# Kernel tuning notes

Hardware: AMD Instinct MI355X
Metric: run time of the kernel (lower is better)

Reference implementation:

```python
import jax, jax.numpy as jnp
import numpy as np

B, T, D = 32, 256, 1024      # batch, seq_len, input_size
H = D // 2                   # LSTM hidden size = 512
K = 128                      # num_tags


def setup_inputs() -> dict:
    key = jax.random.key(0)
    ks = jax.random.split(key, 16)
    s_in = 1.0 / np.sqrt(D + K)
    s_h = 1.0 / np.sqrt(H)
    return {
        "hiddens": jax.random.normal(ks[0], (B, T, D), jnp.float32),
        "h_t": jax.random.normal(ks[1], (2, B, H), jnp.float32),
        "c_t": jax.random.normal(ks[2], (2, B, H), jnp.float32),
        "mask": jnp.ones((B, T), jnp.float32),
        # output layer: Linear(H, K)
        "W_out": jax.random.normal(ks[3], (K, H), jnp.float32) * s_h,
        "b_out": jnp.zeros((K,), jnp.float32),
        # LSTM layer 0: input dim = K + D
        "W_ih0": jax.random.normal(ks[4], (4 * H, K + D), jnp.float32) * s_in,
        "W_hh0": jax.random.normal(ks[5], (4 * H, H), jnp.float32) * s_h,
        "b_ih0": jnp.zeros((4 * H,), jnp.float32),
        "b_hh0": jnp.zeros((4 * H,), jnp.float32),
        # LSTM layer 1: input dim = H
        "W_ih1": jax.random.normal(ks[6], (4 * H, H), jnp.float32) * s_h,
        "W_hh1": jax.random.normal(ks[7], (4 * H, H), jnp.float32) * s_h,
        "b_ih1": jnp.zeros((4 * H,), jnp.float32),
        "b_hh1": jnp.zeros((4 * H,), jnp.float32),
    }


def _lstm_cell(x, h, c, W_ih, W_hh, b_ih, b_hh):
    g = x @ W_ih.T + h @ W_hh.T + b_ih + b_hh
    i, f, gg, o = jnp.split(g, 4, axis=-1)
    i = jax.nn.sigmoid(i); f = jax.nn.sigmoid(f)
    gg = jnp.tanh(gg); o = jax.nn.sigmoid(o)
    c = f * c + i * gg
    h = o * jnp.tanh(c)
    return h, c


def reference(hiddens, h_t, c_t, mask, W_out, b_out,
              W_ih0, W_hh0, b_ih0, b_hh0, W_ih1, W_hh1, b_ih1, b_hh1):
    # initial previous-tag distribution from first frame's first half
    last_tag = hiddens[:, 0, :H] @ W_out.T + b_out          # [B,K]
    sm = jax.nn.softmax(last_tag, axis=-1)

    def step(carry, x_t):
        h1, c1, h2, c2, sm = carry
        inp = jnp.concatenate([x_t, sm], axis=-1)           # [B, D+K]
        h1, c1 = _lstm_cell(inp, h1, c1, W_ih0, W_hh0, b_ih0, b_hh0)
        h2, c2 = _lstm_cell(h1, h2, c2, W_ih1, W_hh1, b_ih1, b_hh1)
        logit = h2 @ W_out.T + b_out                        # [B,K]
        sm = jax.nn.softmax(logit, axis=-1)
        return (h1, c1, h2, c2, sm), logit

    carry0 = (h_t[0], c_t[0], h_t[1], c_t[1], sm)
    _, logits_t = jax.lax.scan(step, carry0, jnp.swapaxes(hiddens, 0, 1))  # [T,B,K]
    logits = jnp.swapaxes(logits_t, 0, 1)                   # [B,T,K]
    logits = logits + (1.0 - mask)[:, :, None] * jnp.float32(-1e32)
    prob = jax.nn.softmax(logits, axis=-1)
    return prob
```

## Files before the change

### kernel.cpp

```cpp
#include <hip/hip_runtime.h>
#include <cstdint>
#include <cstddef>


#define Bz   32
#define Tz   256
#define Dz   1024
#define Hz   512
#define NK   128
#define IN0  1152
#define NBLK 256
#define BH   16384

typedef float vf4 __attribute__((ext_vector_type(4)));

__device__ __forceinline__ void ldsc4(vf4& d, const float* p) {
  asm volatile("global_load_dwordx4 %0, %1, off sc0 sc1" : "=v"(d) : "v"(p));
}
__device__ __forceinline__ void stsc1(float* p, float v) {
  asm volatile("global_store_dword %0, %1, off sc0 sc1" :: "v"(p), "v"(v) : "memory");
}
#define FENCE8(c, a0,a1,a2,a3,a4,a5,a6,a7) \
  asm volatile("s_waitcnt vmcnt(" #c ")" : "+v"(a0),"+v"(a1),"+v"(a2),"+v"(a3), \
               "+v"(a4),"+v"(a5),"+v"(a6),"+v"(a7) :: "memory")

#define FMA4(acc, W_, A_) \
  acc = fmaf((W_).x,(A_).x, fmaf((W_).y,(A_).y, fmaf((W_).z,(A_).z, fmaf((W_).w,(A_).w,(acc)))))

__device__ __forceinline__ float sigf(float x) { return 1.0f / (1.0f + expf(-x)); }

__device__ __forceinline__ void gbar(unsigned int* bar, unsigned int g) {
  asm volatile("s_waitcnt vmcnt(0)" ::: "memory");
  __syncthreads();
  if (threadIdx.x == 0)
    __hip_atomic_store(bar + blockIdx.x * 16, g,
                       __ATOMIC_RELAXED, __HIP_MEMORY_SCOPE_SYSTEM);
  if (blockIdx.x == NBLK - 1) {
    unsigned int* wsl = bar + threadIdx.x * 16;
    while (__hip_atomic_load(wsl, __ATOMIC_RELAXED, __HIP_MEMORY_SCOPE_SYSTEM) < g)
      __builtin_amdgcn_s_sleep(1);
    __syncthreads();
    if (threadIdx.x == 0) {
      asm volatile("s_waitcnt vmcnt(0)" ::: "memory");
      __hip_atomic_store(bar + NBLK * 16, g,
                         __ATOMIC_RELAXED, __HIP_MEMORY_SCOPE_SYSTEM);
    }
  } else if (threadIdx.x == 0) {
    while (__hip_atomic_load(bar + NBLK * 16, __ATOMIC_RELAXED,
                             __HIP_MEMORY_SCOPE_SYSTEM) < g)
      __builtin_amdgcn_s_sleep(1);
  }
  __syncthreads();
}

#define FMAROW(r, AV, BASE, KOFF) \
  { vf4 wv = *(const vf4*)&BASE[r][KOFF]; FMA4(A##r, wv, AV); }
#define R16A(OP, AV, BASE, KOFF) \
  OP(0,AV,BASE,KOFF) OP(1,AV,BASE,KOFF) OP(2,AV,BASE,KOFF) OP(3,AV,BASE,KOFF) \
  OP(4,AV,BASE,KOFF) OP(5,AV,BASE,KOFF) OP(6,AV,BASE,KOFF) OP(7,AV,BASE,KOFF) \
  OP(8,AV,BASE,KOFF) OP(9,AV,BASE,KOFF) OP(10,AV,BASE,KOFF) OP(11,AV,BASE,KOFF) \
  OP(12,AV,BASE,KOFF) OP(13,AV,BASE,KOFF) OP(14,AV,BASE,KOFF) OP(15,AV,BASE,KOFF)

#define RED16 { \
  { const bool hi = (ks & 1) != 0; \
    float s0=hi?A0:A8, s1=hi?A1:A9, s2=hi?A2:A10, s3=hi?A3:A11; \
    float s4=hi?A4:A12, s5=hi?A5:A13, s6=hi?A6:A14, s7=hi?A7:A15; \
    float k0=hi?A8:A0, k1=hi?A9:A1, k2=hi?A10:A2, k3=hi?A11:A3; \
    float k4=hi?A12:A4, k5=hi?A13:A5, k6=hi?A14:A6, k7=hi?A15:A7; \
    A0=k0+__shfl_xor(s0,1,64); A1=k1+__shfl_xor(s1,1,64); \
    A2=k2+__shfl_xor(s2,1,64); A3=k3+__shfl_xor(s3,1,64); \
    A4=k4+__shfl_xor(s4,1,64); A5=k5+__shfl_xor(s5,1,64); \
    A6=k6+__shfl_xor(s6,1,64); A7=k7+__shfl_xor(s7,1,64); } \
  { const bool hi = (ks & 2) != 0; \
    float s0=hi?A0:A4, s1=hi?A1:A5, s2=hi?A2:A6, s3=hi?A3:A7; \
    float k0=hi?A4:A0, k1=hi?A5:A1, k2=hi?A6:A2, k3=hi?A7:A3; \
    A0=k0+__shfl_xor(s0,2,64); A1=k1+__shfl_xor(s1,2,64); \
    A2=k2+__shfl_xor(s2,2,64); A3=k3+__shfl_xor(s3,2,64); } \
  { const bool hi = (ks & 4) != 0; \
    float s0=hi?A0:A2, s1=hi?A1:A3; float k0=hi?A2:A0, k1=hi?A3:A1; \
    A0=k0+__shfl_xor(s0,4,64); A1=k1+__shfl_xor(s1,4,64); } \
  { const bool hi = (ks & 8) != 0; \
    float s0=hi?A0:A1; float k0=hi?A1:A0; \
    A0=k0+__shfl_xor(s0,8,64); } }

#define ZERO16 A0=0.f;A1=0.f;A2=0.f;A3=0.f;A4=0.f;A5=0.f;A6=0.f;A7=0.f; \
               A8=0.f;A9=0.f;A10=0.f;A11=0.f;A12=0.f;A13=0.f;A14=0.f;A15=0.f;

#define GATES(CREG, HDST) \
  __syncthreads(); \
  if (tid < 64) { \
    float gi = gbuf[cu][cbl],      gf = gbuf[4 + cu][cbl]; \
    float gg = gbuf[8 + cu][cbl],  go = gbuf[12 + cu][cbl]; \
    CREG = sigf(gf) * CREG + sigf(gi) * tanhf(gg); \
    stsc1(HDST + (size_t)(pg * 16 + cbl) * Hz + jg * 4 + cu, \
          sigf(go) * tanhf(CREG)); \
  }

__device__ void c_slot(const float* src, int t, int bb,
                       const float* __restrict__ W_out, const float* __restrict__ b_out,
                       const float* __restrict__ mask,
                       float* __restrict__ smg, float* __restrict__ out,
                       float (*cpart)[2], float* wred) {
  const int tid = threadIdx.x;
  const int n = tid & 127, kh = tid >> 7;
  float p = 0.0f;
  const float* w  = W_out + (size_t)n * Hz + kh * 256;
  const float* s2 = src + kh * 256;
  #pragma unroll 8
  for (int k = 0; k < 256; k += 4) {
    vf4 sv = *(const vf4*)(s2 + k);
    vf4 wv = *(const vf4*)(w + k);
    p += sv.x * wv.x + sv.y * wv.y + sv.z * wv.z + sv.w * wv.w;
  }
  cpart[n][kh] = p;
  __syncthreads();
  float logit = 0.0f;
  if (tid < 128) logit = cpart[n][0] + cpart[n][1] + b_out[n];
  float m = logit;
  #pragma unroll
  for (int off = 32; off >= 1; off >>= 1) m = fmaxf(m, __shfl_xor(m, off));
  if ((tid & 63) == 0 && tid < 128) wred[tid >> 6] = m;
  __syncthreads();
  float M = fmaxf(wred[0], wred[1]);
  float e = (tid < 128) ? expf(logit - M) : 0.0f;
  float s = e;
  #pragma unroll
  for (int off = 32; off >= 1; off >>= 1) s += __shfl_xor(s, off);
  if ((tid & 63) == 0 && tid < 128) wred[2 + (tid >> 6)] = s;
  __syncthreads();
  float S = wred[2] + wred[3];
  if (tid < 128) stsc1(smg + bb * NK + n, e / S);
  if (t >= 0) {
    float mk = (tid < 128) ? mask[bb * Tz + t] : 1.0f;
    float lm = (tid < 128) ? (logit + (1.0f - mk) * (-1e32f)) : -3.0e38f;
    float m2 = lm;
    #pragma unroll
    for (int off = 32; off >= 1; off >>= 1) m2 = fmaxf(m2, __shfl_xor(m2, off));
    if ((tid & 63) == 0 && tid < 128) wred[4 + (tid >> 6)] = m2;
    __syncthreads();
    float M2 = fmaxf(wred[4], wred[5]);
    float e2 = (tid < 128) ? expf(lm - M2) : 0.0f;
    float s2r = e2;
    #pragma unroll
    for (int off = 32; off >= 1; off >>= 1) s2r += __shfl_xor(s2r, off);
    if ((tid & 63) == 0 && tid < 128) wred[6 + (tid >> 6)] = s2r;
    __syncthreads();
    float S2 = wred[6] + wred[7];
    if (tid < 128) out[((size_t)bb * Tz + t) * NK + n] = e2 / S2;
  }
}

__global__ void __launch_bounds__(256)
xpre_kernel(const float* __restrict__ hiddens, const float* __restrict__ W_ih0,
            const float* __restrict__ b_ih0, const float* __restrict__ b_hh0,
            float* __restrict__ Xpre, int t0, int colTiles, int cstride) {
  __shared__ float Ws[16][64];
  __shared__ float Hs[16][64];
  const int tid = threadIdx.x;
  const int bx = blockIdx.x % colTiles;
  const int by = blockIdx.x / colTiles;
  const int n0 = by * 64, c0 = bx * 64;
  const int tx = tid & 15, ty = tid >> 4;
  const int ldn = tid >> 2;
  const int ldk = (tid & 3) * 4;

  const int bb = ldn & 31;
  const int tt = t0 + (c0 >> 5) + (ldn >> 5);
  const float* hsrc = hiddens + ((size_t)bb * Tz + tt) * Dz + ldk;
  const float* wsrc = W_ih0 + (size_t)(n0 + ldn) * IN0 + ldk;

  float acc[4][4] = {};
  vf4 wv = *(const vf4*)(wsrc);
  vf4 hv = *(const vf4*)(hsrc);
  for (int k0 = 0; k0 < Dz; k0 += 16) {
    __syncthreads();
    Ws[ldk + 0][ldn] = wv.x; Ws[ldk + 1][ldn] = wv.y;
    Ws[ldk + 2][ldn] = wv.z; Ws[ldk + 3][ldn] = wv.w;
    Hs[ldk + 0][ldn] = hv.x; Hs[ldk + 1][ldn] = hv.y;
    Hs[ldk + 2][ldn] = hv.z; Hs[ldk + 3][ldn] = hv.w;
    __syncthreads();
    if (k0 + 16 < Dz) {
      wv = *(const vf4*)(wsrc + k0 + 16);
      hv = *(const vf4*)(hsrc + k0 + 16);
    }
    #pragma unroll
    for (int k = 0; k < 16; ++k) {
      vf4 a4 = *(const vf4*)&Ws[k][ty * 4];
      vf4 b4 = *(const vf4*)&Hs[k][tx * 4];
      acc[0][0] += a4.x * b4.x; acc[0][1] += a4.x * b4.y; acc[0][2] += a4.x * b4.z; acc[0][3] += a4.x * b4.w;
      acc[1][0] += a4.y * b4.x; acc[1][1] += a4.y * b4.y; acc[1][2] += a4.y * b4.z; acc[1][3] += a4.y * b4.w;
      acc[2][0] += a4.z * b4.x; acc[2][1] += a4.z * b4.y; acc[2][2] += a4.z * b4.z; acc[2][3] += a4.z * b4.w;
      acc[3][0] += a4.w * b4.x; acc[3][1] += a4.w * b4.y; acc[3][2] += a4.w * b4.z; acc[3][3] += a4.w * b4.w;
    }
  }
  #pragma unroll
  for (int i = 0; i < 4; ++i) {
    int n = n0 + ty * 4 + i;
    float bi = b_ih0[n] + b_hh0[n];
    vf4 v; v.x = acc[i][0] + bi; v.y = acc[i][1] + bi;
    v.z = acc[i][2] + bi; v.w = acc[i][3] + bi;
    *(vf4*)(Xpre + (size_t)n * cstride + c0 + tx * 4) = v;
  }
}

__global__ void __launch_bounds__(256)
seq_kernel(const float* __restrict__ hiddens,
           const float* __restrict__ h_t, const float* __restrict__ c_t,
           const float* __restrict__ mask,
           const float* __restrict__ W_out, const float* __restrict__ b_out,
           const float* __restrict__ W_ih0, const float* __restrict__ W_hh0,
           const float* __restrict__ W_ih1, const float* __restrict__ W_hh1,
           const float* __restrict__ b_ih1, const float* __restrict__ b_hh1,
           const float* __restrict__ Xpre, float* __restrict__ out,
           float* __restrict__ h1g, float* __restrict__ h2g,
           float* __restrict__ smg, float* __restrict__ c1g, float* __restrict__ c2g,
           unsigned int* bar, int t0, int nsteps, int cstride) {
  __shared__ float wA[16][640];
  __shared__ float wB[16][1024];
  __shared__ float gbuf[16][17];
  __shared__ float biasB[16];
  __shared__ float hsg[512];
  __shared__ float cpart[128][2];
  __shared__ float wred[8];

  const int tid = threadIdx.x;
  const int bid = blockIdx.x;
  const int jg  = bid >> 1;
  const int pg  = bid & 1;
  const int ks  = tid & 15;
  const int bbl = tid >> 4;
  const int bbg = pg * 16 + bbl;
  const int ks4 = ks * 4;
  const int cu  = tid & 3, cbl = tid >> 2;
  const int rr  = ((ks & 1) << 3) | ((ks & 2) << 1) | ((ks & 4) >> 1) | ((ks & 8) >> 3);
  const int rowG = ((rr >> 2) * Hz) + jg * 4 + (rr & 3);

  for (int r = 0; r < 16; ++r) {
    const int row = ((r >> 2) * Hz) + jg * 4 + (r & 3);
    if (tid * 4 < 512)
      *(vf4*)&wA[r][tid * 4] = *(const vf4*)(W_hh0 + (size_t)row * Hz + tid * 4);
    if (tid * 4 < 128)
      *(vf4*)&wA[r][512 + tid * 4] = *(const vf4*)(W_ih0 + (size_t)row * IN0 + 1024 + tid * 4);
    if (tid * 4 < 512) {
      *(vf4*)&wB[r][tid * 4]       = *(const vf4*)(W_ih1 + (size_t)row * Hz + tid * 4);
      *(vf4*)&wB[r][512 + tid * 4] = *(const vf4*)(W_hh1 + (size_t)row * Hz + tid * 4);
    }
  }
  if (tid < 16) {
    const int row = ((tid >> 2) * Hz) + jg * 4 + (tid & 3);
    biasB[tid] = b_ih1[row] + b_hh1[row];
  }

  float c1r = 0.0f, c2r = 0.0f;
  if (tid < 64) {
    const size_t ci = (size_t)(pg * 16 + cbl) * Hz + jg * 4 + cu;
    if (t0 == 0) { c1r = c_t[ci]; c2r = c_t[BH + ci]; }
    else         { c1r = c1g[ci]; c2r = c2g[ci]; }
  }

  if (t0 == 0) {
    if (bid < 32 && tid < 128) {
      vf4 v1 = *(const vf4*)(h_t + (size_t)bid * Hz + tid * 4);
      vf4 v2 = *(const vf4*)(h_t + BH + (size_t)bid * Hz + tid * 4);
      float* d1 = h1g + BH + (size_t)bid * Hz + tid * 4;
      float* d2 = h2g + BH + (size_t)bid * Hz + tid * 4;
      stsc1(d1, v1.x); stsc1(d1 + 1, v1.y); stsc1(d1 + 2, v1.z); stsc1(d1 + 3, v1.w);
      stsc1(d2, v2.x); stsc1(d2 + 1, v2.y); stsc1(d2 + 2, v2.z); stsc1(d2 + 3, v2.w);
    }
    if (bid < 32) {
      if (tid < 128)
        *(vf4*)&hsg[tid * 4] = *(const vf4*)(hiddens + (size_t)bid * Tz * Dz + tid * 4);
      __syncthreads();
      c_slot(hsg, -1, bid, W_out, b_out, mask, smg, out, cpart, wred);
    }
  }
  __syncthreads();
  unsigned int g = 1;
  gbar(bar, g); ++g;

  for (int t = t0; t < t0 + nsteps; ++t) {
    const float* h1prev = h1g + ((t + 1) & 1) * BH;
    float*       h1cur  = h1g + (t & 1) * BH;
    const float* h2prev = h2g + ((t + 1) & 1) * BH;
    float*       h2cur  = h2g + (t & 1) * BH;
    float A0,A1,A2,A3,A4,A5,A6,A7,A8,A9,A10,A11,A12,A13,A14,A15;

    {
      vf4 ah0,ah1,ah2,ah3,ah4,ah5,ah6,ah7, as0,as1;
      const float* hp = h1prev + (size_t)bbg * Hz + ks4;
      ldsc4(ah0, hp);        ldsc4(ah1, hp + 64);  ldsc4(ah2, hp + 128);
      ldsc4(ah3, hp + 192);  ldsc4(ah4, hp + 256); ldsc4(ah5, hp + 320);
      ldsc4(ah6, hp + 384);  ldsc4(ah7, hp + 448);
      const float* sp = smg + (size_t)bbg * NK + ks4;
      ldsc4(as0, sp);        ldsc4(as1, sp + 64);
      float xv = Xpre[(size_t)rowG * cstride + (t - t0) * 32 + bbg];
      ZERO16
      FENCE8(3, ah0,ah1,ah2,ah3,ah4,ah5,ah6,ah7);
      R16A(FMAROW, ah0, wA, ks4 +   0)
      R16A(FMAROW, ah1, wA, ks4 +  64)
      R16A(FMAROW, ah2, wA, ks4 + 128)
      R16A(FMAROW, ah3, wA, ks4 + 192)
      R16A(FMAROW, ah4, wA, ks4 + 256)
      R16A(FMAROW, ah5, wA, ks4 + 320)
      R16A(FMAROW, ah6, wA, ks4 + 384)
      R16A(FMAROW, ah7, wA, ks4 + 448)
      asm volatile("s_waitcnt vmcnt(0)" : "+v"(as0), "+v"(as1), "+v"(xv) :: "memory");
      R16A(FMAROW, as0, wA, ks4 + 512)
      R16A(FMAROW, as1, wA, ks4 + 576)
      RED16
      gbuf[rr][bbl] = A0 + xv;
      GATES(c1r, h1cur)
    }
    gbar(bar, g); ++g;

    {
      vf4 aa0,aa1,aa2,aa3,aa4,aa5,aa6,aa7, ab0,ab1,ab2,ab3,ab4,ab5,ab6,ab7;
      const float* p1 = h1cur + (size_t)bbg * Hz + ks4;
      ldsc4(aa0, p1);       ldsc4(aa1, p1 + 64);  ldsc4(aa2, p1 + 128);
      ldsc4(aa3, p1 + 192); ldsc4(aa4, p1 + 256); ldsc4(aa5, p1 + 320);
      ldsc4(aa6, p1 + 384); ldsc4(aa7, p1 + 448);
      const float* p2 = h2prev + (size_t)bbg * Hz + ks4;
      ldsc4(ab0, p2);       ldsc4(ab1, p2 + 64);  ldsc4(ab2, p2 + 128);
      ldsc4(ab3, p2 + 192); ldsc4(ab4, p2 + 256); ldsc4(ab5, p2 + 320);
      ldsc4(ab6, p2 + 384); ldsc4(ab7, p2 + 448);
      ZERO16
      FENCE8(8, aa0,aa1,aa2,aa3,aa4,aa5,aa6,aa7);
      R16A(FMAROW, aa0, wB, ks4 +   0)
      R16A(FMAROW, aa1, wB, ks4 +  64)
      R16A(FMAROW, aa2, wB, ks4 + 128)
      R16A(FMAROW, aa3, wB, ks4 + 192)
      R16A(FMAROW, aa4, wB, ks4 + 256)
      R16A(FMAROW, aa5, wB, ks4 + 320)
      R16A(FMAROW, aa6, wB, ks4 + 384)
      R16A(FMAROW, aa7, wB, ks4 + 448)
      FENCE8(0, ab0,ab1,ab2,ab3,ab4,ab5,ab6,ab7);
      R16A(FMAROW, ab0, wB, ks4 + 512)
      R16A(FMAROW, ab1, wB, ks4 + 576)
      R16A(FMAROW, ab2, wB, ks4 + 640)
      R16A(FMAROW, ab3, wB, ks4 + 704)
      R16A(FMAROW, ab4, wB, ks4 + 768)
      R16A(FMAROW, ab5, wB, ks4 + 832)
      R16A(FMAROW, ab6, wB, ks4 + 896)
      R16A(FMAROW, ab7, wB, ks4 + 960)
      RED16
      gbuf[rr][bbl] = A0 + biasB[rr];
      GATES(c2r, h2cur)
    }
    gbar(bar, g); ++g;

    if (bid < 32) {
      if (tid < 128) {
        vf4 v;
        ldsc4(v, h2cur + (size_t)bid * Hz + tid * 4);
        asm volatile("s_waitcnt vmcnt(0)" : "+v"(v) :: "memory");
        *(vf4*)&hsg[tid * 4] = v;
      }
      __syncthreads();
      c_slot(hsg, t, bid, W_out, b_out, mask, smg, out, cpart, wred);
    }
    gbar(bar, g); ++g;
  }

  if (tid < 64) {
    const size_t ci = (size_t)(pg * 16 + cbl) * Hz + jg * 4 + cu;
    stsc1(c1g + ci, c1r);
    stsc1(c2g + ci, c2r);
  }
}

extern "C" void kernel_launch(void* const* d_in, const int* in_sizes, int n_in,
                              void* d_out, int out_size, void* d_ws, size_t ws_size,
                              hipStream_t stream) {
  (void)in_sizes; (void)n_in; (void)out_size;
  const float* hiddens = (const float*)d_in[0];
  const float* h_t     = (const float*)d_in[1];
  const float* c_t     = (const float*)d_in[2];
  const float* mask    = (const float*)d_in[3];
  const float* W_out   = (const float*)d_in[4];
  const float* b_out   = (const float*)d_in[5];
  const float* W_ih0   = (const float*)d_in[6];
  const float* W_hh0   = (const float*)d_in[7];
  const float* b_ih0   = (const float*)d_in[8];
  const float* b_hh0   = (const float*)d_in[9];
  const float* W_ih1   = (const float*)d_in[10];
  const float* W_hh1   = (const float*)d_in[11];
  const float* b_ih1   = (const float*)d_in[12];
  const float* b_hh1   = (const float*)d_in[13];
  float* out = (float*)d_out;

  unsigned int* bar = (unsigned int*)d_ws;
  float* base = (float*)((char*)d_ws + 32768);
  float* h1g  = base;
  float* h2g  = h1g + 2 * BH;
  float* smg  = h2g + 2 * BH;
  float* c1g  = smg + Bz * NK;
  float* c2g  = c1g + BH;
  float* Xpre = c2g + BH;

  const size_t fullNeed = 32768 + (size_t)(102400 + 2048 * 8192) * 4;
  const bool full = ws_size >= fullNeed;
  const int NCH    = full ? 1 : 16;
  const int CH     = full ? Tz : 16;
  const int cstr   = full ? (Tz * 32) : (16 * 32);
  const int cTiles = cstr / 64;

  for (int c = 0; c < NCH; ++c) {
    const int t0 = c * CH;
    hipMemsetAsync(bar, 0, 32768, stream);
    hipLaunchKernelGGL(xpre_kernel, dim3(32 * cTiles), dim3(256), 0, stream,
                       hiddens, W_ih0, b_ih0, b_hh0, Xpre, t0, cTiles, cstr);
    int nsteps = CH, cs = cstr, tt0 = t0;
    void* ka[] = { (void*)&hiddens, (void*)&h_t, (void*)&c_t, (void*)&mask,
                   (void*)&W_out, (void*)&b_out, (void*)&W_ih0, (void*)&W_hh0,
                   (void*)&W_ih1, (void*)&W_hh1, (void*)&b_ih1, (void*)&b_hh1,
                   (void*)&Xpre, (void*)&out, (void*)&h1g, (void*)&h2g,
                   (void*)&smg, (void*)&c1g, (void*)&c2g, (void*)&bar,
                   (void*)&tt0, (void*)&nsteps, (void*)&cs };
    hipError_t err = hipLaunchCooperativeKernel((void*)seq_kernel, dim3(NBLK),
                                                dim3(256), ka, 0, stream);
    if (err != hipSuccess) {
      hipLaunchKernelGGL(seq_kernel, dim3(NBLK), dim3(256), 0, stream,
                         hiddens, h_t, c_t, mask, W_out, b_out, W_ih0, W_hh0,
                         W_ih1, W_hh1, b_ih1, b_hh1, Xpre, out,
                         h1g, h2g, smg, c1g, c2g, bar, tt0, nsteps, cs);
    }
  }
}
```

Before: 6.131 ms.

## Split grid barrier by batch half and overlap output stage via per-batch flags

The centralized grid barrier is replaced with a decentralized barrier over the 128 blocks of each batch half: every block polls per-block slots with vector loads, so no single master block relays. The third barrier per timestep, the one around the output and softmax stage, is removed. That stage now runs at the start of the next step for the previous h2 and signals a per-batch flag, which layer-0 waits on just before it reads the softmax input. The h2prev loads are hoisted into layer 0 so they overlap the layer-0 compute, and the layer-1 FMA order is swapped. This trades barrier latency for added polling traffic and more subtle ordering, with the final output step moved after the loop.

```diff
diff --git a/kernel.cpp b/kernel.cpp
--- a/kernel.cpp
+++ b/kernel.cpp
@@ -13,11 +13,18 @@
 #define BH   16384
 
 typedef float vf4 __attribute__((ext_vector_type(4)));
+typedef unsigned int uv4 __attribute__((ext_vector_type(4)));
 
 __device__ __forceinline__ void ldsc4(vf4& d, const float* p) {
   asm volatile("global_load_dwordx4 %0, %1, off sc0 sc1" : "=v"(d) : "v"(p));
 }
+__device__ __forceinline__ void ldg1(float& d, const float* p) {
+  asm volatile("global_load_dword %0, %1, off" : "=v"(d) : "v"(p));
+}
 __device__ __forceinline__ void stsc1(float* p, float v) {
+  asm volatile("global_store_dword %0, %1, off sc0 sc1" :: "v"(p), "v"(v) : "memory");
+}
+__device__ __forceinline__ void stsc1u(unsigned int* p, unsigned int v) {
   asm volatile("global_store_dword %0, %1, off sc0 sc1" :: "v"(p), "v"(v) : "memory");
 }
 #define FENCE8(c, a0,a1,a2,a3,a4,a5,a6,a7) \
@@ -29,26 +36,20 @@
 
 __device__ __forceinline__ float sigf(float x) { return 1.0f / (1.0f + expf(-x)); }
 
-__device__ __forceinline__ void gbar(unsigned int* bar, unsigned int g) {
+__device__ __forceinline__ void gbar(unsigned int* slots, unsigned int g) {
   asm volatile("s_waitcnt vmcnt(0)" ::: "memory");
   __syncthreads();
-  if (threadIdx.x == 0)
-    __hip_atomic_store(bar + blockIdx.x * 16, g,
-                       __ATOMIC_RELAXED, __HIP_MEMORY_SCOPE_SYSTEM);
-  if (blockIdx.x == NBLK - 1) {
-    unsigned int* wsl = bar + threadIdx.x * 16;
-    while (__hip_atomic_load(wsl, __ATOMIC_RELAXED, __HIP_MEMORY_SCOPE_SYSTEM) < g)
+  const int tid = threadIdx.x;
+  if (tid == 0) stsc1u(slots + (blockIdx.x >> 1), g);
+  if (tid < 64) {
+    const unsigned int* p = slots + (tid & 31) * 4;
+    for (;;) {
+      uv4 v;
+      asm volatile("global_load_dwordx4 %0, %1, off sc0 sc1" : "=v"(v) : "v"(p));
+      asm volatile("s_waitcnt vmcnt(0)" : "+v"(v) :: "memory");
+      if (__all(v.x >= g && v.y >= g && v.z >= g && v.w >= g)) break;
       __builtin_amdgcn_s_sleep(1);
-    __syncthreads();
-    if (threadIdx.x == 0) {
-      asm volatile("s_waitcnt vmcnt(0)" ::: "memory");
-      __hip_atomic_store(bar + NBLK * 16, g,
-                         __ATOMIC_RELAXED, __HIP_MEMORY_SCOPE_SYSTEM);
-    }
-  } else if (threadIdx.x == 0) {
-    while (__hip_atomic_load(bar + NBLK * 16, __ATOMIC_RELAXED,
-                             __HIP_MEMORY_SCOPE_SYSTEM) < g)
-      __builtin_amdgcn_s_sleep(1);
+    }
   }
   __syncthreads();
 }
@@ -100,7 +101,8 @@
                        const float* __restrict__ W_out, const float* __restrict__ b_out,
                        const float* __restrict__ mask,
                        float* __restrict__ smg, float* __restrict__ out,
-                       float (*cpart)[2], float* wred) {
+                       float (*cpart)[2], float* wred,
+                       unsigned int* smflag, unsigned int fval) {
   const int tid = threadIdx.x;
   const int n = tid & 127, kh = tid >> 7;
   float p = 0.0f;
@@ -130,6 +132,9 @@
   __syncthreads();
   float S = wred[2] + wred[3];
   if (tid < 128) stsc1(smg + bb * NK + n, e / S);
+  asm volatile("s_waitcnt vmcnt(0)" ::: "memory");
+  __syncthreads();
+  if (fval && tid == 0) stsc1u(smflag, fval);
   if (t >= 0) {
     float mk = (tid < 128) ? mask[bb * Tz + t] : 1.0f;
     float lm = (tid < 128) ? (logit + (1.0f - mk) * (-1e32f)) : -3.0e38f;
@@ -234,6 +239,10 @@
   const int cu  = tid & 3, cbl = tid >> 2;
   const int rr  = ((ks & 1) << 3) | ((ks & 2) << 1) | ((ks & 4) >> 1) | ((ks & 8) >> 3);
   const int rowG = ((rr >> 2) * Hz) + jg * 4 + (rr & 3);
+  const int hb = ((bid & 1) << 4) | (bid >> 1);
+
+  unsigned int* barg = bar + pg * 512;
+  unsigned int* smf  = bar + 4096;
 
   for (int r = 0; r < 16; ++r) {
     const int row = ((r >> 2) * Hz) + jg * 4 + (r & 3);
@@ -260,23 +269,24 @@
 
   if (t0 == 0) {
     if (bid < 32 && tid < 128) {
-      vf4 v1 = *(const vf4*)(h_t + (size_t)bid * Hz + tid * 4);
-      vf4 v2 = *(const vf4*)(h_t + BH + (size_t)bid * Hz + tid * 4);
-      float* d1 = h1g + BH + (size_t)bid * Hz + tid * 4;
-      float* d2 = h2g + BH + (size_t)bid * Hz + tid * 4;
+      vf4 v1 = *(const vf4*)(h_t + (size_t)hb * Hz + tid * 4);
+      vf4 v2 = *(const vf4*)(h_t + BH + (size_t)hb * Hz + tid * 4);
+      float* d1 = h1g + BH + (size_t)hb * Hz + tid * 4;
+      float* d2 = h2g + BH + (size_t)hb * Hz + tid * 4;
       stsc1(d1, v1.x); stsc1(d1 + 1, v1.y); stsc1(d1 + 2, v1.z); stsc1(d1 + 3, v1.w);
       stsc1(d2, v2.x); stsc1(d2 + 1, v2.y); stsc1(d2 + 2, v2.z); stsc1(d2 + 3, v2.w);
     }
     if (bid < 32) {
       if (tid < 128)
-        *(vf4*)&hsg[tid * 4] = *(const vf4*)(hiddens + (size_t)bid * Tz * Dz + tid * 4);
+        *(vf4*)&hsg[tid * 4] = *(const vf4*)(hiddens + (size_t)hb * Tz * Dz + tid * 4);
       __syncthreads();
-      c_slot(hsg, -1, bid, W_out, b_out, mask, smg, out, cpart, wred);
+      c_slot(hsg, -1, hb, W_out, b_out, mask, smg, out, cpart, wred,
+             smf + hb * 16, 0u);
     }
   }
   __syncthreads();
   unsigned int g = 1;
-  gbar(bar, g); ++g;
+  gbar(barg, g); ++g;
 
   for (int t = t0; t < t0 + nsteps; ++t) {
     const float* h1prev = h1g + ((t + 1) & 1) * BH;
@@ -284,18 +294,34 @@
     const float* h2prev = h2g + ((t + 1) & 1) * BH;
     float*       h2cur  = h2g + (t & 1) * BH;
     float A0,A1,A2,A3,A4,A5,A6,A7,A8,A9,A10,A11,A12,A13,A14,A15;
+    vf4 ab0,ab1,ab2,ab3,ab4,ab5,ab6,ab7;
 
     {
+      if (bid < 32 && t > t0) {
+        if (tid < 128) {
+          vf4 v;
+          ldsc4(v, h2prev + (size_t)hb * Hz + tid * 4);
+          asm volatile("s_waitcnt vmcnt(0)" : "+v"(v) :: "memory");
+          *(vf4*)&hsg[tid * 4] = v;
+        }
+        __syncthreads();
+        c_slot(hsg, t - 1, hb, W_out, b_out, mask, smg, out, cpart, wred,
+               smf + hb * 16, (unsigned int)(t - t0 + 1));
+      }
+
       vf4 ah0,ah1,ah2,ah3,ah4,ah5,ah6,ah7, as0,as1;
       const float* hp = h1prev + (size_t)bbg * Hz + ks4;
       ldsc4(ah0, hp);        ldsc4(ah1, hp + 64);  ldsc4(ah2, hp + 128);
       ldsc4(ah3, hp + 192);  ldsc4(ah4, hp + 256); ldsc4(ah5, hp + 320);
       ldsc4(ah6, hp + 384);  ldsc4(ah7, hp + 448);
-      const float* sp = smg + (size_t)bbg * NK + ks4;
-      ldsc4(as0, sp);        ldsc4(as1, sp + 64);
-      float xv = Xpre[(size_t)rowG * cstride + (t - t0) * 32 + bbg];
+      const float* p2 = h2prev + (size_t)bbg * Hz + ks4;
+      ldsc4(ab0, p2);       ldsc4(ab1, p2 + 64);  ldsc4(ab2, p2 + 128);
+      ldsc4(ab3, p2 + 192); ldsc4(ab4, p2 + 256); ldsc4(ab5, p2 + 320);
+      ldsc4(ab6, p2 + 384); ldsc4(ab7, p2 + 448);
+      float xv;
+      ldg1(xv, Xpre + (size_t)rowG * cstride + (t - t0) * 32 + bbg);
       ZERO16
-      FENCE8(3, ah0,ah1,ah2,ah3,ah4,ah5,ah6,ah7);
+      FENCE8(9, ah0,ah1,ah2,ah3,ah4,ah5,ah6,ah7);
       R16A(FMAROW, ah0, wA, ks4 +   0)
       R16A(FMAROW, ah1, wA, ks4 +  64)
       R16A(FMAROW, ah2, wA, ks4 + 128)
@@ -304,6 +330,17 @@
       R16A(FMAROW, ah5, wA, ks4 + 320)
       R16A(FMAROW, ah6, wA, ks4 + 384)
       R16A(FMAROW, ah7, wA, ks4 + 448)
+      if (t > t0) {
+        const unsigned int* fp = smf + bbg * 16;
+        const unsigned int tgt = (unsigned int)(t - t0 + 1);
+        unsigned int fv;
+        do {
+          asm volatile("global_load_dword %0, %1, off sc0 sc1" : "=v"(fv) : "v"(fp));
+          asm volatile("s_waitcnt vmcnt(0)" : "+v"(fv) :: "memory");
+        } while (fv < tgt);
+      }
+      const float* sp = smg + (size_t)bbg * NK + ks4;
+      ldsc4(as0, sp);        ldsc4(as1, sp + 64);
       asm volatile("s_waitcnt vmcnt(0)" : "+v"(as0), "+v"(as1), "+v"(xv) :: "memory");
       R16A(FMAROW, as0, wA, ks4 + 512)
       R16A(FMAROW, as1, wA, ks4 + 576)
@@ -311,28 +348,15 @@
       gbuf[rr][bbl] = A0 + xv;
       GATES(c1r, h1cur)
     }
-    gbar(bar, g); ++g;
+    gbar(barg, g); ++g;
 
     {
-      vf4 aa0,aa1,aa2,aa3,aa4,aa5,aa6,aa7, ab0,ab1,ab2,ab3,ab4,ab5,ab6,ab7;
+      vf4 aa0,aa1,aa2,aa3,aa4,aa5,aa6,aa7;
       const float* p1 = h1cur + (size_t)bbg * Hz + ks4;
       ldsc4(aa0, p1);       ldsc4(aa1, p1 + 64);  ldsc4(aa2, p1 + 128);
       ldsc4(aa3, p1 + 192); ldsc4(aa4, p1 + 256); ldsc4(aa5, p1 + 320);
       ldsc4(aa6, p1 + 384); ldsc4(aa7, p1 + 448);
-      const float* p2 = h2prev + (size_t)bbg * Hz + ks4;
-      ldsc4(ab0, p2);       ldsc4(ab1, p2 + 64);  ldsc4(ab2, p2 + 128);
-      ldsc4(ab3, p2 + 192); ldsc4(ab4, p2 + 256); ldsc4(ab5, p2 + 320);
-      ldsc4(ab6, p2 + 384); ldsc4(ab7, p2 + 448);
       ZERO16
-      FENCE8(8, aa0,aa1,aa2,aa3,aa4,aa5,aa6,aa7);
-      R16A(FMAROW, aa0, wB, ks4 +   0)
-      R16A(FMAROW, aa1, wB, ks4 +  64)
-      R16A(FMAROW, aa2, wB, ks4 + 128)
-      R16A(FMAROW, aa3, wB, ks4 + 192)
-      R16A(FMAROW, aa4, wB, ks4 + 256)
-      R16A(FMAROW, aa5, wB, ks4 + 320)
-      R16A(FMAROW, aa6, wB, ks4 + 384)
-      R16A(FMAROW, aa7, wB, ks4 + 448)
       FENCE8(0, ab0,ab1,ab2,ab3,ab4,ab5,ab6,ab7);
       R16A(FMAROW, ab0, wB, ks4 + 512)
       R16A(FMAROW, ab1, wB, ks4 + 576)
@@ -342,23 +366,36 @@
       R16A(FMAROW, ab5, wB, ks4 + 832)
       R16A(FMAROW, ab6, wB, ks4 + 896)
       R16A(FMAROW, ab7, wB, ks4 + 960)
+      FENCE8(0, aa0,aa1,aa2,aa3,aa4,aa5,aa6,aa7);
+      R16A(FMAROW, aa0, wB, ks4 +   0)
+      R16A(FMAROW, aa1, wB, ks4 +  64)
+      R16A(FMAROW, aa2, wB, ks4 + 128)
+      R16A(FMAROW, aa3, wB, ks4 + 192)
+      R16A(FMAROW, aa4, wB, ks4 + 256)
+      R16A(FMAROW, aa5, wB, ks4 + 320)
+      R16A(FMAROW, aa6, wB, ks4 + 384)
+      R16A(FMAROW, aa7, wB, ks4 + 448)
       RED16
       gbuf[rr][bbl] = A0 + biasB[rr];
       GATES(c2r, h2cur)
     }
-    gbar(bar, g); ++g;
-
+    gbar(barg, g); ++g;
+  }
+
+  {
+    const int tl = t0 + nsteps - 1;
+    const float* h2last = h2g + (tl & 1) * BH;
     if (bid < 32) {
       if (tid < 128) {
         vf4 v;
-        ldsc4(v, h2cur + (size_t)bid * Hz + tid * 4);
+        ldsc4(v, h2last + (size_t)hb * Hz + tid * 4);
         asm volatile("s_waitcnt vmcnt(0)" : "+v"(v) :: "memory");
         *(vf4*)&hsg[tid * 4] = v;
       }
       __syncthreads();
-      c_slot(hsg, t, bid, W_out, b_out, mask, smg, out, cpart, wred);
-    }
-    gbar(bar, g); ++g;
+      c_slot(hsg, tl, hb, W_out, b_out, mask, smg, out, cpart, wred,
+             smf + hb * 16, 0u);
+    }
   }
 
   if (tid < 64) {
```

Result: slower. 9.419 ms (+53.6%).

## Split grid barrier into two independent batch-half groups of 128 blocks

Applied to the files above, without the earlier changes.

Each block works only on one half of the batch (pg = bid & 1), so the single 256-block grid barrier is replaced by two independent barriers, one per batch half, each with 128 slots and its own master and broadcast word. The output-slot work is remapped (hb) so that the blocks handling a batch row are in the same group as the blocks that produce it. The aim is to halve the number of arrivals each master polls and to let the two halves proceed without waiting on each other. The risk is extra barrier memory and added complexity in the index mapping.

```diff
diff --git a/kernel.cpp b/kernel.cpp
--- a/kernel.cpp
+++ b/kernel.cpp
@@ -29,25 +29,26 @@
 
 __device__ __forceinline__ float sigf(float x) { return 1.0f / (1.0f + expf(-x)); }
 
-__device__ __forceinline__ void gbar(unsigned int* bar, unsigned int g) {
+__device__ __forceinline__ void gbar(unsigned int* slots, unsigned int* bcast,
+                                     int gidx, bool master, unsigned int g) {
   asm volatile("s_waitcnt vmcnt(0)" ::: "memory");
   __syncthreads();
   if (threadIdx.x == 0)
-    __hip_atomic_store(bar + blockIdx.x * 16, g,
+    __hip_atomic_store(slots + gidx * 16, g,
                        __ATOMIC_RELAXED, __HIP_MEMORY_SCOPE_SYSTEM);
-  if (blockIdx.x == NBLK - 1) {
-    unsigned int* wsl = bar + threadIdx.x * 16;
-    while (__hip_atomic_load(wsl, __ATOMIC_RELAXED, __HIP_MEMORY_SCOPE_SYSTEM) < g)
-      __builtin_amdgcn_s_sleep(1);
+  if (master) {
+    if (threadIdx.x < 128) {
+      unsigned int* wsl = slots + threadIdx.x * 16;
+      while (__hip_atomic_load(wsl, __ATOMIC_RELAXED, __HIP_MEMORY_SCOPE_SYSTEM) < g)
+        __builtin_amdgcn_s_sleep(1);
+    }
     __syncthreads();
     if (threadIdx.x == 0) {
       asm volatile("s_waitcnt vmcnt(0)" ::: "memory");
-      __hip_atomic_store(bar + NBLK * 16, g,
-                         __ATOMIC_RELAXED, __HIP_MEMORY_SCOPE_SYSTEM);
+      __hip_atomic_store(bcast, g, __ATOMIC_RELAXED, __HIP_MEMORY_SCOPE_SYSTEM);
     }
   } else if (threadIdx.x == 0) {
-    while (__hip_atomic_load(bar + NBLK * 16, __ATOMIC_RELAXED,
-                             __HIP_MEMORY_SCOPE_SYSTEM) < g)
+    while (__hip_atomic_load(bcast, __ATOMIC_RELAXED, __HIP_MEMORY_SCOPE_SYSTEM) < g)
       __builtin_amdgcn_s_sleep(1);
   }
   __syncthreads();
@@ -234,7 +235,14 @@
   const int cu  = tid & 3, cbl = tid >> 2;
   const int rr  = ((ks & 1) << 3) | ((ks & 2) << 1) | ((ks & 4) >> 1) | ((ks & 8) >> 3);
   const int rowG = ((rr >> 2) * Hz) + jg * 4 + (rr & 3);
-
+  const int hb = ((bid & 1) << 4) | (bid >> 1);
+
+  unsigned int* barg = bar + pg * 2048;
+  unsigned int* bcst = bar + 4096 + pg * 16;
+  const int  gidx    = bid >> 1;
+  const bool gmaster = (gidx == 127);
+
+  #pragma clang loop unroll(disable)
   for (int r = 0; r < 16; ++r) {
     const int row = ((r >> 2) * Hz) + jg * 4 + (r & 3);
     if (tid * 4 < 512)
@@ -260,24 +268,25 @@
 
   if (t0 == 0) {
     if (bid < 32 && tid < 128) {
-      vf4 v1 = *(const vf4*)(h_t + (size_t)bid * Hz + tid * 4);
-      vf4 v2 = *(const vf4*)(h_t + BH + (size_t)bid * Hz + tid * 4);
-      float* d1 = h1g + BH + (size_t)bid * Hz + tid * 4;
-      float* d2 = h2g + BH + (size_t)bid * Hz + tid * 4;
+      vf4 v1 = *(const vf4*)(h_t + (size_t)hb * Hz + tid * 4);
+      vf4 v2 = *(const vf4*)(h_t + BH + (size_t)hb * Hz + tid * 4);
+      float* d1 = h1g + BH + (size_t)hb * Hz + tid * 4;
+      float* d2 = h2g + BH + (size_t)hb * Hz + tid * 4;
       stsc1(d1, v1.x); stsc1(d1 + 1, v1.y); stsc1(d1 + 2, v1.z); stsc1(d1 + 3, v1.w);
       stsc1(d2, v2.x); stsc1(d2 + 1, v2.y); stsc1(d2 + 2, v2.z); stsc1(d2 + 3, v2.w);
     }
     if (bid < 32) {
       if (tid < 128)
-        *(vf4*)&hsg[tid * 4] = *(const vf4*)(hiddens + (size_t)bid * Tz * Dz + tid * 4);
+        *(vf4*)&hsg[tid * 4] = *(const vf4*)(hiddens + (size_t)hb * Tz * Dz + tid * 4);
       __syncthreads();
-      c_slot(hsg, -1, bid, W_out, b_out, mask, smg, out, cpart, wred);
+      c_slot(hsg, -1, hb, W_out, b_out, mask, smg, out, cpart, wred);
     }
   }
   __syncthreads();
   unsigned int g = 1;
-  gbar(bar, g); ++g;
-
+  gbar(barg, bcst, gidx, gmaster, g); ++g;
+
+  #pragma clang loop unroll(disable)
   for (int t = t0; t < t0 + nsteps; ++t) {
     const float* h1prev = h1g + ((t + 1) & 1) * BH;
     float*       h1cur  = h1g + (t & 1) * BH;
@@ -311,7 +320,7 @@
       gbuf[rr][bbl] = A0 + xv;
       GATES(c1r, h1cur)
     }
-    gbar(bar, g); ++g;
+    gbar(barg, bcst, gidx, gmaster, g); ++g;
 
     {
       vf4 aa0,aa1,aa2,aa3,aa4,aa5,aa6,aa7, ab0,ab1,ab2,ab3,ab4,ab5,ab6,ab7;
@@ -346,19 +355,19 @@
       gbuf[rr][bbl] = A0 + biasB[rr];
       GATES(c2r, h2cur)
     }
-    gbar(bar, g); ++g;
+    gbar(barg, bcst, gidx, gmaster, g); ++g;
 
     if (bid < 32) {
       if (tid < 128) {
         vf4 v;
-        ldsc4(v, h2cur + (size_t)bid * Hz + tid * 4);
+        ldsc4(v, h2cur + (size_t)hb * Hz + tid * 4);
         asm volatile("s_waitcnt vmcnt(0)" : "+v"(v) :: "memory");
         *(vf4*)&hsg[tid * 4] = v;
       }
       __syncthreads();
-      c_slot(hsg, t, bid, W_out, b_out, mask, smg, out, cpart, wred);
-    }
-    gbar(bar, g); ++g;
+      c_slot(hsg, t, hb, W_out, b_out, mask, smg, out, cpart, wred);
+    }
+    gbar(barg, bcst, gidx, gmaster, g); ++g;
   }
 
   if (tid < 64) {
```

Result: faster. 5.992 ms (-2.3%).
